# Performance work log

Measured on AMD Instinct MI355X. Metric: run time of the kernel, lower is better.

## Reference

```python
import jax, jax.numpy as jnp
import numpy as np

D_IN = 768
D_OUT = 768
SEQ = 4096


def setup_inputs() -> dict:
    key = jax.random.key(0)
    kx, kq, kk, kv = jax.random.split(key, 4)
    # nn.Linear weight shape is [d_out, d_in]; kaiming-uniform-ish scale
    s = 1.0 / np.sqrt(D_IN)
    return {
        "x": jax.random.normal(kx, (SEQ, D_IN), dtype=jnp.float32),
        "Wq": jax.random.uniform(kq, (D_OUT, D_IN), jnp.float32, -s, s),
        "Wk": jax.random.uniform(kk, (D_OUT, D_IN), jnp.float32, -s, s),
        "Wv": jax.random.uniform(kv, (D_OUT, D_IN), jnp.float32, -s, s),
    }


def reference(x, Wq, Wk, Wv):
    # queries/keys/values: [S, d_out] = x @ W.T
    q = x @ Wq.T
    k = x @ Wk.T
    v = x @ Wv.T
    scale = 1.0 / jnp.sqrt(jnp.asarray(k.shape[-1], x.dtype))
    scores = (q @ k.T) * scale               # [S, S]
    attn = jax.nn.softmax(scores, axis=-1)   # [S, S]
    return attn @ v                          # [S, d_out]
```

## Files before the change

kernel.cpp:

```cpp
#include <hip/hip_runtime.h>
#include <hip/hip_bf16.h>

using bf16 = __hip_bfloat16;
typedef __attribute__((ext_vector_type(4))) float f32x4;
typedef __attribute__((ext_vector_type(8))) short short8;

#define SEQ 4096
#define DIM 768


__global__ void convert_all_kernel(const float* __restrict__ x,
                                   const float* __restrict__ wq,
                                   const float* __restrict__ wk,
                                   const float* __restrict__ wv,
                                   bf16* __restrict__ xc, bf16* __restrict__ wqc,
                                   bf16* __restrict__ wkc, bf16* __restrict__ wvc) {
  const int XB = (SEQ * DIM) / 2048;
  const int WB = (DIM * DIM) / 2048;
  int b = blockIdx.x;
  const float* src; bf16* dst; int off;
  if (b < XB)               { src = x;  dst = xc;  off = b * 2048; }
  else if (b < XB + WB)     { src = wq; dst = wqc; off = (b - XB) * 2048; }
  else if (b < XB + 2 * WB) { src = wk; dst = wkc; off = (b - XB - WB) * 2048; }
  else                      { src = wv; dst = wvc; off = (b - XB - 2 * WB) * 2048; }
  int i = off + threadIdx.x * 8;
  float4 f0 = *(const float4*)(src + i);
  float4 f1 = *(const float4*)(src + i + 4);
  bf16 tmp[8];
  tmp[0] = __float2bfloat16(f0.x); tmp[1] = __float2bfloat16(f0.y);
  tmp[2] = __float2bfloat16(f0.z); tmp[3] = __float2bfloat16(f0.w);
  tmp[4] = __float2bfloat16(f1.x); tmp[5] = __float2bfloat16(f1.y);
  tmp[6] = __float2bfloat16(f1.z); tmp[7] = __float2bfloat16(f1.w);
  *(uint4*)(dst + i) = *(const uint4*)tmp;
}


__device__ __forceinline__ void gload_lds16(const bf16* g, bf16* l) {
  __builtin_amdgcn_global_load_lds(
      (const __attribute__((address_space(1))) void*)g,
      (__attribute__((address_space(3))) void*)l,
      16, 0, 0);
}

__device__ __forceinline__ void stage64(const bf16* g, int ldk, bf16* l,
                                        int wave, int lane) {
  int r = lane >> 2;
  int c = (lane & 3) * 8;
  const bf16* gw = g + (size_t)(wave * 32) * ldk;
  bf16* lw = l + wave * 1024;
#pragma unroll
  for (int h = 0; h < 2; h++)
#pragma unroll
    for (int s = 0; s < 2; s++)
      gload_lds16(gw + (size_t)(s * 16 + r) * ldk + h * 32 + c,
                  lw + h * 4096 + s * 512);
}

__device__ __forceinline__ void gemm_core(const bf16* __restrict__ A,
                                          const bf16* __restrict__ B,
                                          int ldk, int klen, int m0, int n0,
                                          f32x4 acc[4][4],
                                          bf16* lA, bf16* lB) {
  const int tid  = threadIdx.x;
  const int wave = tid >> 6, lane = tid & 63;
  const int wm = (wave & 1) * 64, wn = (wave >> 1) * 64;
  const int g = lane >> 4, lr = lane & 15;
  const bf16* Abase = A + (size_t)m0 * ldk;
  const bf16* Bbase = B + (size_t)n0 * ldk;
  for (int kk = 0; kk < klen; kk += 64) {
    stage64(Abase + kk, ldk, lA, wave, lane);
    stage64(Bbase + kk, ldk, lB, wave, lane);
    __syncthreads();
#pragma unroll
    for (int h = 0; h < 2; h++) {
      short8 af[4], bfr[4];
#pragma unroll
      for (int i = 0; i < 4; i++)
        af[i] = *(const short8*)&lA[h * 4096 + (wm + i * 16 + lr) * 32 + g * 8];
#pragma unroll
      for (int j = 0; j < 4; j++)
        bfr[j] = *(const short8*)&lB[h * 4096 + (wn + j * 16 + lr) * 32 + g * 8];
#pragma unroll
      for (int i = 0; i < 4; i++)
#pragma unroll
        for (int j = 0; j < 4; j++)
          acc[i][j] = __builtin_amdgcn_mfma_f32_16x16x32_bf16(af[i], bfr[j], acc[i][j], 0, 0, 0);
    }
    __syncthreads();
  }
}


__global__ __launch_bounds__(256, 3) void qkv_kernel(
    const bf16* __restrict__ x, const bf16* __restrict__ Wq,
    const bf16* __restrict__ Wk, const bf16* __restrict__ Wv,
    bf16* __restrict__ Q, bf16* __restrict__ Kb, bf16* __restrict__ Vt) {
  __shared__ __align__(16) bf16 lA[2 * 128 * 32];
  __shared__ __align__(16) bf16 lB[2 * 128 * 32];
  const int m0  = blockIdx.x * 128;
  const int n0g = blockIdx.y * 128;
  const int wsel = n0g / DIM;
  const int n0   = n0g % DIM;
  const bf16* W = (wsel == 0) ? Wq : (wsel == 1) ? Wk : Wv;
  f32x4 acc[4][4] = {};
  gemm_core(x, W, DIM, DIM, m0, n0, acc, lA, lB);

  const int tid = threadIdx.x, wave = tid >> 6, lane = tid & 63;
  const int wm = (wave & 1) * 64, wn = (wave >> 1) * 64;
  const int g = lane >> 4, lr = lane & 15;
  const float scale = 0.03608439182435161f;
#pragma unroll
  for (int i = 0; i < 4; i++)
#pragma unroll
    for (int j = 0; j < 4; j++)
#pragma unroll
      for (int r = 0; r < 4; r++) {
        int row = m0 + wm + i * 16 + g * 4 + r;
        int col = n0 + wn + j * 16 + lr;
        float v = acc[i][j][r];
        if (wsel == 0)      Q[row * DIM + col]  = __float2bfloat16(v * scale);
        else if (wsel == 1) Kb[row * DIM + col] = __float2bfloat16(v);
        else                Vt[col * SEQ + row] = __float2bfloat16(v);
      }
}

__global__ __launch_bounds__(256, 3) void score_kernel(
    const bf16* __restrict__ Q, const bf16* __restrict__ Kb,
    bf16* __restrict__ P, float* __restrict__ denom) {
  __shared__ __align__(16) bf16 lA[2 * 128 * 32];
  __shared__ __align__(16) bf16 lB[2 * 128 * 32];
  const int m0 = blockIdx.x * 128;
  const int n0 = blockIdx.y * 128;
  f32x4 acc[4][4] = {};
  gemm_core(Q, Kb, DIM, DIM, m0, n0, acc, lA, lB);

  const int tid = threadIdx.x, wave = tid >> 6, lane = tid & 63;
  const int wm = (wave & 1) * 64, wn = (wave >> 1) * 64;
  const int g = lane >> 4, lr = lane & 15;
#pragma unroll
  for (int i = 0; i < 4; i++) {
    float rsum[4] = {0.f, 0.f, 0.f, 0.f};
#pragma unroll
    for (int j = 0; j < 4; j++)
#pragma unroll
      for (int r = 0; r < 4; r++) {
        float p = __expf(acc[i][j][r]);
        int row = m0 + wm + i * 16 + g * 4 + r;
        int col = n0 + wn + j * 16 + lr;
        P[row * SEQ + col] = __float2bfloat16(p);
        rsum[r] += p;
      }
#pragma unroll
    for (int r = 0; r < 4; r++) {
      float s = rsum[r];
      s += __shfl_xor(s, 1);
      s += __shfl_xor(s, 2);
      s += __shfl_xor(s, 4);
      s += __shfl_xor(s, 8);
      if (lr == 0) atomicAdd(&denom[m0 + wm + i * 16 + g * 4 + r], s);
    }
  }
}

__global__ __launch_bounds__(256, 3) void pv_kernel(
    const bf16* __restrict__ P, const bf16* __restrict__ Vt,
    float* __restrict__ partial) {
  __shared__ __align__(16) bf16 lA[2 * 128 * 32];
  __shared__ __align__(16) bf16 lB[2 * 128 * 32];
  const int m0 = blockIdx.x * 128;
  const int n0 = blockIdx.y * 128;
  const int kbase = blockIdx.z * (SEQ / 4);
  f32x4 acc[4][4] = {};
  gemm_core(P + kbase, Vt + kbase, SEQ, SEQ / 4, m0, n0, acc, lA, lB);

  float* pout = partial + (size_t)blockIdx.z * SEQ * DIM;
  const int tid = threadIdx.x, wave = tid >> 6, lane = tid & 63;
  const int wm = (wave & 1) * 64, wn = (wave >> 1) * 64;
  const int g = lane >> 4, lr = lane & 15;
#pragma unroll
  for (int i = 0; i < 4; i++)
#pragma unroll
    for (int j = 0; j < 4; j++)
#pragma unroll
      for (int r = 0; r < 4; r++) {
        int row = m0 + wm + i * 16 + g * 4 + r;
        int col = n0 + wn + j * 16 + lr;
        pout[row * DIM + col] = acc[i][j][r];
      }
}

__global__ __launch_bounds__(256) void reduce_kernel(
    const float* __restrict__ partial, const float* __restrict__ denom,
    float* __restrict__ out) {
  const size_t stride = (size_t)SEQ * DIM;
  int i = (blockIdx.x * 256 + threadIdx.x) * 4;
  float4 s0 = *(const float4*)(partial + i);
  float4 s1 = *(const float4*)(partial + stride + i);
  float4 s2 = *(const float4*)(partial + 2 * stride + i);
  float4 s3 = *(const float4*)(partial + 3 * stride + i);
  float inv = 1.0f / denom[i / DIM];
  float4 o;
  o.x = (s0.x + s1.x + s2.x + s3.x) * inv;
  o.y = (s0.y + s1.y + s2.y + s3.y) * inv;
  o.z = (s0.z + s1.z + s2.z + s3.z) * inv;
  o.w = (s0.w + s1.w + s2.w + s3.w) * inv;
  *(float4*)(out + i) = o;
}

extern "C" void kernel_launch(void* const* d_in, const int* in_sizes, int n_in,
                              void* d_out, int out_size, void* d_ws, size_t ws_size,
                              hipStream_t stream) {
  const float* x_raw  = (const float*)d_in[0];
  const float* Wq_raw = (const float*)d_in[1];
  const float* Wk_raw = (const float*)d_in[2];
  const float* Wv_raw = (const float*)d_in[3];
  float* out = (float*)d_out;

  bf16* xc  = (bf16*)d_ws;
  bf16* Wqc = xc  + (size_t)SEQ * DIM;
  bf16* Wkc = Wqc + (size_t)DIM * DIM;
  bf16* Wvc = Wkc + (size_t)DIM * DIM;
  bf16* Q   = Wvc + (size_t)DIM * DIM;
  bf16* Kb  = Q   + (size_t)SEQ * DIM;
  bf16* Vt  = Kb  + (size_t)SEQ * DIM;
  bf16* P   = Vt  + (size_t)DIM * SEQ;
  float* denom   = (float*)(P + (size_t)SEQ * SEQ);
  float* partial = denom + SEQ;

  const int nx = SEQ * DIM;
  const int nw = DIM * DIM;
  const int conv_blocks = nx / 2048 + 3 * (nw / 2048);

  hipMemsetAsync(denom, 0, SEQ * sizeof(float), stream);
  convert_all_kernel<<<conv_blocks, 256, 0, stream>>>(
      x_raw, Wq_raw, Wk_raw, Wv_raw, xc, Wqc, Wkc, Wvc);
  qkv_kernel<<<dim3(SEQ / 128, 2304 / 128), 256, 0, stream>>>(xc, Wqc, Wkc, Wvc, Q, Kb, Vt);
  score_kernel<<<dim3(SEQ / 128, SEQ / 128), 256, 0, stream>>>(Q, Kb, P, denom);
  pv_kernel<<<dim3(SEQ / 128, DIM / 128, 4), 256, 0, stream>>>(P, Vt, partial);
  reduce_kernel<<<nx / 4 / 256, 256, 0, stream>>>(partial, denom, out);
}
```

Before: 176.8 us.

## Transpose V through LDS, store PV partials in bf16, fold denom zeroing into convert

The V projection epilogue now stages the tile in padded shared memory and writes the transposed Vt with coalesced 16-byte stores instead of scattered 2-byte strided stores. The split-K PV partials are stored as bf16 instead of fp32, which halves partial write and reduce read traffic, and the reduce kernel now handles 8 elements per thread. The denominator memset is folded into the convert kernel to remove one enqueue. Storing partials in bf16 adds rounding error to the final sum.

```diff
diff --git a/kernel.cpp b/kernel.cpp
--- a/kernel.cpp
+++ b/kernel.cpp
@@ -14,10 +14,17 @@
                                    const float* __restrict__ wk,
                                    const float* __restrict__ wv,
                                    bf16* __restrict__ xc, bf16* __restrict__ wqc,
-                                   bf16* __restrict__ wkc, bf16* __restrict__ wvc) {
+                                   bf16* __restrict__ wkc, bf16* __restrict__ wvc,
+                                   float* __restrict__ denom) {
   const int XB = (SEQ * DIM) / 2048;
   const int WB = (DIM * DIM) / 2048;
   int b = blockIdx.x;
+  if (b == 0) {
+    float4 z = {0.f, 0.f, 0.f, 0.f};
+#pragma unroll
+    for (int q = 0; q < 4; q++)
+      *(float4*)(denom + (threadIdx.x * 4 + q * 1024)) = z;
+  }
   const float* src; bf16* dst; int off;
   if (b < XB)               { src = x;  dst = xc;  off = b * 2048; }
   else if (b < XB + WB)     { src = wq; dst = wqc; off = (b - XB) * 2048; }
@@ -34,7 +41,6 @@
   *(uint4*)(dst + i) = *(const uint4*)tmp;
 }
 
-
 __device__ __forceinline__ void gload_lds16(const bf16* g, bf16* l) {
   __builtin_amdgcn_global_load_lds(
       (const __attribute__((address_space(1))) void*)g,
@@ -95,8 +101,9 @@
     const bf16* __restrict__ x, const bf16* __restrict__ Wq,
     const bf16* __restrict__ Wk, const bf16* __restrict__ Wv,
     bf16* __restrict__ Q, bf16* __restrict__ Kb, bf16* __restrict__ Vt) {
-  __shared__ __align__(16) bf16 lA[2 * 128 * 32];
-  __shared__ __align__(16) bf16 lB[2 * 128 * 32];
+  __shared__ __align__(16) bf16 smem[16384];
+  bf16* lA = smem;
+  bf16* lB = smem + 8192;
   const int m0  = blockIdx.x * 128;
   const int n0g = blockIdx.y * 128;
   const int wsel = n0g / DIM;
@@ -109,26 +116,55 @@
   const int wm = (wave & 1) * 64, wn = (wave >> 1) * 64;
   const int g = lane >> 4, lr = lane & 15;
   const float scale = 0.03608439182435161f;
-#pragma unroll
-  for (int i = 0; i < 4; i++)
-#pragma unroll
-    for (int j = 0; j < 4; j++)
-#pragma unroll
-      for (int r = 0; r < 4; r++) {
-        int row = m0 + wm + i * 16 + g * 4 + r;
-        int col = n0 + wn + j * 16 + lr;
-        float v = acc[i][j][r];
-        if (wsel == 0)      Q[row * DIM + col]  = __float2bfloat16(v * scale);
-        else if (wsel == 1) Kb[row * DIM + col] = __float2bfloat16(v);
-        else                Vt[col * SEQ + row] = __float2bfloat16(v);
+
+  if (wsel == 2) {
+    bf16* tile = smem;
+#pragma unroll
+    for (int ph = 0; ph < 2; ph++) {
+      __syncthreads();
+      if ((wave >> 1) == ph) {
+#pragma unroll
+        for (int i = 0; i < 4; i++)
+#pragma unroll
+          for (int j = 0; j < 4; j++)
+#pragma unroll
+            for (int r = 0; r < 4; r++)
+              tile[(wm + i * 16 + g * 4 + r) * 67 + j * 16 + lr] =
+                  __float2bfloat16(acc[i][j][r]);
       }
+      __syncthreads();
+      int cl = tid >> 2;
+      int r0 = (tid & 3) * 32;
+      bf16 vals[32];
+#pragma unroll
+      for (int k = 0; k < 32; k++) vals[k] = tile[(r0 + k) * 67 + cl];
+      bf16* dst = Vt + (size_t)(n0 + ph * 64 + cl) * SEQ + m0 + r0;
+#pragma unroll
+      for (int q = 0; q < 4; q++)
+        *(uint4*)(dst + q * 8) = *(const uint4*)(vals + q * 8);
+    }
+  } else {
+    bf16* dstm = (wsel == 0) ? Q : Kb;
+    float fs = (wsel == 0) ? scale : 1.0f;
+#pragma unroll
+    for (int i = 0; i < 4; i++)
+#pragma unroll
+      for (int j = 0; j < 4; j++)
+#pragma unroll
+        for (int r = 0; r < 4; r++) {
+          int row = m0 + wm + i * 16 + g * 4 + r;
+          int col = n0 + wn + j * 16 + lr;
+          dstm[row * DIM + col] = __float2bfloat16(acc[i][j][r] * fs);
+        }
+  }
 }
 
 __global__ __launch_bounds__(256, 3) void score_kernel(
     const bf16* __restrict__ Q, const bf16* __restrict__ Kb,
     bf16* __restrict__ P, float* __restrict__ denom) {
-  __shared__ __align__(16) bf16 lA[2 * 128 * 32];
-  __shared__ __align__(16) bf16 lB[2 * 128 * 32];
+  __shared__ __align__(16) bf16 smem[16384];
+  bf16* lA = smem;
+  bf16* lB = smem + 8192;
   const int m0 = blockIdx.x * 128;
   const int n0 = blockIdx.y * 128;
   f32x4 acc[4][4] = {};
@@ -164,16 +200,17 @@
 
 __global__ __launch_bounds__(256, 3) void pv_kernel(
     const bf16* __restrict__ P, const bf16* __restrict__ Vt,
-    float* __restrict__ partial) {
-  __shared__ __align__(16) bf16 lA[2 * 128 * 32];
-  __shared__ __align__(16) bf16 lB[2 * 128 * 32];
+    bf16* __restrict__ partial) {
+  __shared__ __align__(16) bf16 smem[16384];
+  bf16* lA = smem;
+  bf16* lB = smem + 8192;
   const int m0 = blockIdx.x * 128;
   const int n0 = blockIdx.y * 128;
   const int kbase = blockIdx.z * (SEQ / 4);
   f32x4 acc[4][4] = {};
   gemm_core(P + kbase, Vt + kbase, SEQ, SEQ / 4, m0, n0, acc, lA, lB);
 
-  float* pout = partial + (size_t)blockIdx.z * SEQ * DIM;
+  bf16* pout = partial + (size_t)blockIdx.z * SEQ * DIM;
   const int tid = threadIdx.x, wave = tid >> 6, lane = tid & 63;
   const int wm = (wave & 1) * 64, wn = (wave >> 1) * 64;
   const int g = lane >> 4, lr = lane & 15;
@@ -185,26 +222,29 @@
       for (int r = 0; r < 4; r++) {
         int row = m0 + wm + i * 16 + g * 4 + r;
         int col = n0 + wn + j * 16 + lr;
-        pout[row * DIM + col] = acc[i][j][r];
+        pout[row * DIM + col] = __float2bfloat16(acc[i][j][r]);
       }
 }
 
 __global__ __launch_bounds__(256) void reduce_kernel(
-    const float* __restrict__ partial, const float* __restrict__ denom,
+    const bf16* __restrict__ partial, const float* __restrict__ denom,
     float* __restrict__ out) {
   const size_t stride = (size_t)SEQ * DIM;
-  int i = (blockIdx.x * 256 + threadIdx.x) * 4;
-  float4 s0 = *(const float4*)(partial + i);
-  float4 s1 = *(const float4*)(partial + stride + i);
-  float4 s2 = *(const float4*)(partial + 2 * stride + i);
-  float4 s3 = *(const float4*)(partial + 3 * stride + i);
+  int i = (blockIdx.x * 256 + threadIdx.x) * 8;
+  uint4 u0 = *(const uint4*)(partial + i);
+  uint4 u1 = *(const uint4*)(partial + stride + i);
+  uint4 u2 = *(const uint4*)(partial + 2 * stride + i);
+  uint4 u3 = *(const uint4*)(partial + 3 * stride + i);
+  bf16 a0[8], a1[8], a2[8], a3[8];
+  *(uint4*)a0 = u0; *(uint4*)a1 = u1; *(uint4*)a2 = u2; *(uint4*)a3 = u3;
   float inv = 1.0f / denom[i / DIM];
-  float4 o;
-  o.x = (s0.x + s1.x + s2.x + s3.x) * inv;
-  o.y = (s0.y + s1.y + s2.y + s3.y) * inv;
-  o.z = (s0.z + s1.z + s2.z + s3.z) * inv;
-  o.w = (s0.w + s1.w + s2.w + s3.w) * inv;
-  *(float4*)(out + i) = o;
+  float o[8];
+#pragma unroll
+  for (int k = 0; k < 8; k++)
+    o[k] = (__bfloat162float(a0[k]) + __bfloat162float(a1[k]) +
+            __bfloat162float(a2[k]) + __bfloat162float(a3[k])) * inv;
+  *(float4*)(out + i)     = *(const float4*)(o);
+  *(float4*)(out + i + 4) = *(const float4*)(o + 4);
 }
 
 extern "C" void kernel_launch(void* const* d_in, const int* in_sizes, int n_in,
@@ -224,18 +264,17 @@
   bf16* Kb  = Q   + (size_t)SEQ * DIM;
   bf16* Vt  = Kb  + (size_t)SEQ * DIM;
   bf16* P   = Vt  + (size_t)DIM * SEQ;
-  float* denom   = (float*)(P + (size_t)SEQ * SEQ);
-  float* partial = denom + SEQ;
+  float* denom  = (float*)(P + (size_t)SEQ * SEQ);
+  bf16* partial = (bf16*)(denom + SEQ);
 
   const int nx = SEQ * DIM;
   const int nw = DIM * DIM;
   const int conv_blocks = nx / 2048 + 3 * (nw / 2048);
 
-  hipMemsetAsync(denom, 0, SEQ * sizeof(float), stream);
   convert_all_kernel<<<conv_blocks, 256, 0, stream>>>(
-      x_raw, Wq_raw, Wk_raw, Wv_raw, xc, Wqc, Wkc, Wvc);
+      x_raw, Wq_raw, Wk_raw, Wv_raw, xc, Wqc, Wkc, Wvc, denom);
   qkv_kernel<<<dim3(SEQ / 128, 2304 / 128), 256, 0, stream>>>(xc, Wqc, Wkc, Wvc, Q, Kb, Vt);
   score_kernel<<<dim3(SEQ / 128, SEQ / 128), 256, 0, stream>>>(Q, Kb, P, denom);
   pv_kernel<<<dim3(SEQ / 128, DIM / 128, 4), 256, 0, stream>>>(P, Vt, partial);
-  reduce_kernel<<<nx / 4 / 256, 256, 0, stream>>>(partial, denom, out);
-}
+  reduce_kernel<<<nx / 8 / 256, 256, 0, stream>>>(partial, denom, out);
+}
```

After: 167.1 us. 1.06x faster.
